# Kernel tuning notes

Hardware: AMD Instinct MI355X
Metric: run time of the kernel (lower is better)

Reference implementation:

```python
import jax, jax.numpy as jnp
import numpy as np

N = 50000
E = 800000
DF = 8        # dim_feat
DH = 32       # dim_hidden = out_channels per head
H = 4         # heads
HC = H * DH
DE = 4        # edge_dim
DD = 256      # dim_dense
DO = 4        # dim_out
NL = 3        # num GAT layers
SLOPE = 0.2   # GAT negative_slope
NL_SLOPE = 0.01  # nn.LeakyReLU default


def setup_inputs() -> dict:
    key = jax.random.key(0)
    ks = jax.random.split(key, 32)
    p = lambda k, shp: (jax.random.normal(k, shp, dtype=jnp.float32) * 0.1)
    inp = {
        "x": jax.random.normal(ks[0], (N, DF), dtype=jnp.float32),
        "edge_index": jax.random.randint(ks[1], (2, E), 0, N, dtype=jnp.int64),
        "edge_attr": jax.random.normal(ks[2], (E, DE), dtype=jnp.float32),
        # layer 0 (in = DF)
        "Wl0": p(ks[3], (DF, HC)), "bl0": jnp.zeros((HC,), jnp.float32),
        "Wr0": p(ks[4], (DF, HC)), "br0": jnp.zeros((HC,), jnp.float32),
        "We0": p(ks[5], (DE, HC)),
        "att0": p(ks[6], (H, DH)),
        "bo0": jnp.zeros((DH,), jnp.float32),
        # layers 1..NL-1 stacked (in = DH)
        "Wl": p(ks[7], (NL - 1, DH, HC)), "bl": jnp.zeros((NL - 1, HC), jnp.float32),
        "Wr": p(ks[8], (NL - 1, DH, HC)), "br": jnp.zeros((NL - 1, HC), jnp.float32),
        "We": p(ks[9], (NL - 1, DE, HC)),
        "att": p(ks[10], (NL - 1, H, DH)),
        "bo": jnp.zeros((NL - 1, DH), jnp.float32),
        # MLP head
        "Wd1": p(ks[11], (DH, DD)), "bd1": jnp.zeros((DD,), jnp.float32),
        "Wd2": p(ks[12], (DD, DO)), "bd2": jnp.zeros((DO,), jnp.float32),
    }
    return inp


def gat_layer(x, src, dst, ea, Wl, bl, Wr, br, We, att, bo):
    # GATv2ConvNorm, concat=False, no self loops, eval (dropout off)
    xl = (x @ Wl + bl).reshape(-1, H, DH)   # source transform  [N,H,C]
    xr = (x @ Wr + br).reshape(-1, H, DH)   # target transform  [N,H,C]
    x_j = xl[src]                            # [E,H,C]
    x_i = xr[dst]                            # [E,H,C]
    ef = (ea @ We).reshape(-1, H, DH)        # [E,H,C]
    m = jax.nn.leaky_relu(x_i + x_j + ef, negative_slope=SLOPE)
    e = jnp.einsum('ehc,hc->eh', m, att)     # logits [E,H]
    # Lipschitz norm on logits
    ni = jnp.linalg.norm(x_i, axis=-1)       # [E,H]
    nj = jnp.linalg.norm(x_j, axis=-1)       # [E,H]
    mx = jax.ops.segment_max(nj, dst, num_segments=N)
    mx = jnp.where(jnp.isfinite(mx), mx, 0.0)  # empty groups -> 0 (torch include_self=False init)
    e = e / (4.0 * (ni + mx[dst]) + 1e-12)
    # scatter softmax over destination groups
    emax = jax.ops.segment_max(e, dst, num_segments=N)
    z = jnp.exp(e - emax[dst])
    s = jax.ops.segment_sum(z, dst, num_segments=N)
    alpha = z / (s[dst] + 1e-16)             # [E,H]
    out = jax.ops.segment_sum(alpha[..., None] * x_j, dst, num_segments=N)  # [N,H,C]
    return out.mean(axis=1) + bo             # concat=False -> mean over heads


def reference(x, edge_index, edge_attr, Wl0, bl0, Wr0, br0, We0, att0, bo0,
              Wl, bl, Wr, br, We, att, bo, Wd1, bd1, Wd2, bd2):
    src, dst = edge_index[0], edge_index[1]
    act = lambda a: jax.nn.leaky_relu(a, negative_slope=NL_SLOPE)
    h = act(gat_layer(x, src, dst, edge_attr, Wl0, bl0, Wr0, br0, We0, att0, bo0))
    for i in range(NL - 1):
        h = act(gat_layer(h, src, dst, edge_attr, Wl[i], bl[i], Wr[i], br[i], We[i], att[i], bo[i]))
    h = act(h @ Wd1 + bd1)
    return h @ Wd2 + bd2
```

## Files before the change

### kernel.cpp

```cpp
#include <hip/hip_runtime.h>
#include <hip/hip_fp16.h>
#include <math.h>

#define NN 50000
#define EE 800000
#define DFi 8
#define DHc 32
#define Hh 4
#define HCc 128
#define DEe 4
#define DDd 256
#define DOo 4
#define NBK 196

__global__ void detect_kernel(const unsigned int* __restrict__ w, int nwords, int* __restrict__ flag) {
    unsigned int acc = 0;
    for (int i = 2 * threadIdx.x + 1; i < nwords; i += 512) acc |= w[i];
    if (acc) atomicOr(flag, 1);
}

__global__ void convert_count_kernel(const void* __restrict__ buf, const int* __restrict__ flag,
                                     int* __restrict__ EI, int* __restrict__ counts,
                                     int* __restrict__ rnk) {
    int i = blockIdx.x * 256 + threadIdx.x;
    if (i >= 2 * EE) return;
    int v = (*flag) ? ((const int*)buf)[i] : (int)(((const long long*)buf)[i]);
    EI[i] = v;
    if (i >= EE) rnk[i - EE] = atomicAdd(&counts[v], 1);
}

__global__ void scanA_kernel(const int* __restrict__ counts, int* __restrict__ roff,
                             int* __restrict__ bsum, int M) {
    __shared__ int sd[256];
    int t = threadIdx.x;
    int idx = blockIdx.x * 256 + t;
    int v = (idx < M) ? counts[idx] : 0;
    sd[t] = v;
    __syncthreads();
    for (int off = 1; off < 256; off <<= 1) {
        int x = (t >= off) ? sd[t - off] : 0;
        __syncthreads();
        sd[t] += x;
        __syncthreads();
    }
    if (idx < M) roff[idx] = sd[t] - v;
    if (t == 255) bsum[blockIdx.x] = sd[255];
}

__global__ void scanB_kernel(const int* __restrict__ bsum, int* __restrict__ boff, int nb) {
    __shared__ int sd[256];
    int t = threadIdx.x;
    int v = (t < nb) ? bsum[t] : 0;
    sd[t] = v;
    __syncthreads();
    for (int off = 1; off < 256; off <<= 1) {
        int x = (t >= off) ? sd[t - off] : 0;
        __syncthreads();
        sd[t] += x;
        __syncthreads();
    }
    boff[t] = sd[t] - v;
}

__global__ void scanC_kernel(int* __restrict__ roff, const int* __restrict__ boff, int M) {
    int idx = blockIdx.x * 256 + threadIdx.x;
    if (idx < M) roff[idx] += boff[idx >> 8];
}

__global__ void fill_kernel(const int* __restrict__ EI, const int* __restrict__ roff,
                            const int* __restrict__ rnk, long long* __restrict__ ce) {
    int e = blockIdx.x * 256 + threadIdx.x;
    if (e >= EE) return;
    int d = EI[EE + e];
    int s = EI[e];
    ce[roff[d] + rnk[e]] = ((long long)e << 32) | (unsigned int)s;
}

__global__ __launch_bounds__(256) void sortw_kernel(const int* __restrict__ roff,
                                                    long long* __restrict__ ce,
                                                    const float4* __restrict__ EA4,
                                                    int* __restrict__ col,
                                                    __half* __restrict__ EAc) {
    const int n = blockIdx.x * 4 + (threadIdx.x >> 6);
    if (n >= NN) return;
    const int lane = threadIdx.x & 63;
    const int a = roff[n];
    const int d = roff[n + 1] - a;
    if (d <= 0) return;
    if (d <= 64) {
        int srcv = 0;
        unsigned key = 0xFFFFFFFFu;
        if (lane < d) {
            long long v = ce[a + lane];
            srcv = (int)(v & 0xffffffffLL);
            unsigned eid = (unsigned)(v >> 32);
            key = (eid << 6) | (unsigned)lane;
        }
#pragma unroll
        for (int k = 2; k <= 64; k <<= 1) {
#pragma unroll
            for (int j = k >> 1; j > 0; j >>= 1) {
                unsigned o = (unsigned)__shfl_xor((int)key, j);
                bool up = ((lane & k) == 0);
                bool lower = ((lane & j) == 0);
                unsigned mn = o < key ? o : key;
                unsigned mx = o < key ? key : o;
                key = (lower == up) ? mn : mx;
            }
        }
        if (lane < d) {
            int ol = (int)(key & 63u);
            int src = __shfl(srcv, ol);
            unsigned eid = key >> 6;
            col[a + lane] = src;
            float4 at = EA4[eid];
            __half2 lo = __floats2half2_rn(at.x, at.y);
            __half2 hi = __floats2half2_rn(at.z, at.w);
            uint2 pk;
            pk.x = *reinterpret_cast<unsigned int*>(&lo);
            pk.y = *reinterpret_cast<unsigned int*>(&hi);
            reinterpret_cast<uint2*>(EAc)[a + lane] = pk;
        }
    } else if (lane == 0) {
        for (int i2 = a + 1; i2 < a + d; i2++) {
            long long kk = ce[i2];
            int j2 = i2 - 1;
            while (j2 >= a && ce[j2] > kk) { ce[j2 + 1] = ce[j2]; j2--; }
            ce[j2 + 1] = kk;
        }
        for (int k = 0; k < d; k++) {
            long long key = ce[a + k];
            int src = (int)(key & 0xffffffffLL);
            int eid = (int)(key >> 32);
            col[a + k] = src;
            float4 at = EA4[eid];
            __half2 lo = __floats2half2_rn(at.x, at.y);
            __half2 hi = __floats2half2_rn(at.z, at.w);
            uint2 pk;
            pk.x = *reinterpret_cast<unsigned int*>(&lo);
            pk.y = *reinterpret_cast<unsigned int*>(&hi);
            reinterpret_cast<uint2*>(EAc)[a + k] = pk;
        }
    }
}

__global__ __launch_bounds__(256) void bhist_kernel(const int* __restrict__ roff, int* __restrict__ gbh) {
    __shared__ int hist[256];
    int t = threadIdx.x;
    hist[t] = 0;
    __syncthreads();
    int n = blockIdx.x * 256 + t;
    if (n < NN) {
        int d = roff[n + 1] - roff[n];
        atomicAdd(&hist[d < 255 ? d : 255], 1);
    }
    __syncthreads();
    gbh[t * NBK + blockIdx.x] = hist[t];
}

__global__ __launch_bounds__(256) void bscan_kernel(int* __restrict__ gbh) {
    __shared__ int sd[256];
    int bin = threadIdx.x;
    int s = 0;
    for (int b = 0; b < NBK; b++) { int v = gbh[bin * NBK + b]; gbh[bin * NBK + b] = s; s += v; }
    int r = 255 - bin;
    sd[r] = s;
    __syncthreads();
    for (int off = 1; off < 256; off <<= 1) {
        int x = (r >= off) ? sd[r - off] : 0;
        __syncthreads();
        sd[r] += x;
        __syncthreads();
    }
    int base = sd[r] - s;
    for (int b = 0; b < NBK; b++) gbh[bin * NBK + b] += base;
}

__global__ __launch_bounds__(256) void bscatter_kernel(const int* __restrict__ roff,
                                                       const int* __restrict__ gbh,
                                                       int* __restrict__ perm) {
    __shared__ int hist[256];
    int t = threadIdx.x;
    hist[t] = 0;
    __syncthreads();
    int n = blockIdx.x * 256 + t;
    if (n < NN) {
        int d = roff[n + 1] - roff[n];
        int bin = d < 255 ? d : 255;
        int lr = atomicAdd(&hist[bin], 1);
        perm[gbh[bin * NBK + blockIdx.x] + lr] = n;
    }
}

template <int IN>
__global__ __launch_bounds__(128) void transform_kernel(
    const float* __restrict__ Xin, const float* __restrict__ Wl, const float* __restrict__ bl,
    const float* __restrict__ Wr, const float* __restrict__ br,
    __half* __restrict__ XLh, __half* __restrict__ XRh,
    float* __restrict__ NLn, float* __restrict__ NRn) {
    const int t = threadIdx.x;
    float wl[IN], wr[IN];
#pragma unroll
    for (int k = 0; k < IN; k++) { wl[k] = Wl[k * HCc + t]; wr[k] = Wr[k * HCc + t]; }
    const float blv = bl[t], brv = br[t];
    __shared__ float xst[16][IN];
    const int nbeg = blockIdx.x * 16;
    for (int idx = t; idx < 16 * IN; idx += 128) {
        int r = idx / IN, cc = idx % IN;
        int n = nbeg + r;
        xst[r][cc] = (n < NN) ? Xin[n * IN + cc] : 0.f;
    }
    __syncthreads();
#pragma unroll 4
    for (int r = 0; r < 16; ++r) {
        int n = nbeg + r;
        if (n >= NN) break;
        float al = blv, ar = brv;
#pragma unroll
        for (int k = 0; k < IN; k++) { float xv = xst[r][k]; al = fmaf(xv, wl[k], al); ar = fmaf(xv, wr[k], ar); }
        XLh[n * HCc + t] = __float2half(al);
        XRh[n * HCc + t] = __float2half(ar);
        float sl = al * al, sr = ar * ar;
#pragma unroll
        for (int msk = 1; msk < 32; msk <<= 1) { sl += __shfl_xor(sl, msk); sr += __shfl_xor(sr, msk); }
        if ((t & 31) == 0) { NLn[n * 4 + (t >> 5)] = sqrtf(sl); NRn[n * 4 + (t >> 5)] = sqrtf(sr); }
    }
}

__device__ inline float4 h8tof4(unsigned int a, unsigned int b) {
    __half2 p0 = *reinterpret_cast<const __half2*>(&a);
    __half2 p1 = *reinterpret_cast<const __half2*>(&b);
    float2 lo = __half22float2(p0), hi = __half22float2(p1);
    return make_float4(lo.x, lo.y, hi.x, hi.y);
}

__global__ __launch_bounds__(256) void gat_kernel(
    const __half* __restrict__ XLh, const __half* __restrict__ XRh,
    const float* __restrict__ NLn, const float* __restrict__ NRn,
    const int* __restrict__ roff, const int* __restrict__ col,
    const __half* __restrict__ EAc, const int* __restrict__ perm,
    const float* __restrict__ We,
    const float* __restrict__ att, const float* __restrict__ bo,
    float* __restrict__ Hout) {
    const int lane = threadIdx.x & 63;
    const int c = lane & 15;
    const int g = lane >> 4;
    const int h = c >> 2;
    const int slot = blockIdx.x * 16 + (threadIdx.x >> 6) * 4 + g;
    if (slot >= NN) return;
    const int i = perm[slot];

    const uint4*  XLu4 = reinterpret_cast<const uint4*>(XLh);
    const uint4*  XRu4 = reinterpret_cast<const uint4*>(XRh);
    const uint2*  EAu2 = reinterpret_cast<const uint2*>(EAc);
    const float4* NL4 = reinterpret_cast<const float4*>(NLn);
    const float4* We4 = reinterpret_cast<const float4*>(We);
    const float4* at4 = reinterpret_cast<const float4*>(att);
    const float4* bo4 = reinterpret_cast<const float4*>(bo);
    float4* Ho4 = reinterpret_cast<float4*>(Hout);

    const int base = roff[i];
    const int deg = roff[i + 1] - base;

    if (deg == 0) {
        if (c < 8) {
            float4 b = bo4[c];
            float4 r;
            r.x = b.x > 0.f ? b.x : 0.01f * b.x;
            r.y = b.y > 0.f ? b.y : 0.01f * b.y;
            r.z = b.z > 0.f ? b.z : 0.01f * b.z;
            r.w = b.w > 0.f ? b.w : 0.01f * b.w;
            Ho4[i * 8 + c] = r;
        }
        return;
    }

    const float4 w0l = We4[2 * c],      w0h = We4[2 * c + 1];
    const float4 w1l = We4[32 + 2 * c], w1h = We4[32 + 2 * c + 1];
    const float4 w2l = We4[64 + 2 * c], w2h = We4[64 + 2 * c + 1];
    const float4 w3l = We4[96 + 2 * c], w3h = We4[96 + 2 * c + 1];
    const float4 atl = at4[2 * c],      ath = at4[2 * c + 1];

    uint4 xiu = XRu4[i * 16 + c];
    const float4 xil = h8tof4(xiu.x, xiu.y), xih = h8tof4(xiu.z, xiu.w);
    float srun = 0.f;
    float4 accl = make_float4(0.f, 0.f, 0.f, 0.f);
    float4 acch = make_float4(0.f, 0.f, 0.f, 0.f);

#define ISSUE(X_, E_, K)                                                          \
    {                                                                             \
        int kc = ((K) < deg) ? (K) : 0;                                           \
        int jx = col[base + kc];                                                  \
        X_ = XLu4[jx * 16 + c];                                                   \
        E_ = EAu2[base + kc];                                                     \
    }
    uint4 xA, xB, xC, xD, xE, xF;
    uint2 eA, eB, eC, eD, eE, eF;
    ISSUE(xA, eA, 0); ISSUE(xB, eB, 1); ISSUE(xC, eC, 2);
    ISSUE(xD, eD, 3); ISSUE(xE, eE, 4); ISSUE(xF, eF, 5);

    float4 mx = make_float4(0.f, 0.f, 0.f, 0.f);
    for (int k = c; k < deg; k += 16) {
        int j = col[base + k];
        float4 nj = NL4[j];
        mx.x = fmaxf(mx.x, nj.x); mx.y = fmaxf(mx.y, nj.y);
        mx.z = fmaxf(mx.z, nj.z); mx.w = fmaxf(mx.w, nj.w);
    }
#pragma unroll
    for (int msk = 1; msk < 16; msk <<= 1) {
        mx.x = fmaxf(mx.x, __shfl_xor(mx.x, msk));
        mx.y = fmaxf(mx.y, __shfl_xor(mx.y, msk));
        mx.z = fmaxf(mx.z, __shfl_xor(mx.z, msk));
        mx.w = fmaxf(mx.w, __shfl_xor(mx.w, msk));
    }
    float mxh = (h == 0) ? mx.x : (h == 1) ? mx.y : (h == 2) ? mx.z : mx.w;
    const float invD = 1.0f / (4.0f * (NRn[i * 4 + h] + mxh) + 1e-12f);

#define BODY(X_, E_, K)                                                           \
    {                                                                             \
        float4 a4 = h8tof4((E_).x, (E_).y);                                       \
        float4 xjl = h8tof4((X_).x, (X_).y);                                      \
        float4 xjh = h8tof4((X_).z, (X_).w);                                      \
        float e0 = a4.x * w0l.x; e0 = fmaf(a4.y, w1l.x, e0);                      \
        e0 = fmaf(a4.z, w2l.x, e0); e0 = fmaf(a4.w, w3l.x, e0);                   \
        float e1 = a4.x * w0l.y; e1 = fmaf(a4.y, w1l.y, e1);                      \
        e1 = fmaf(a4.z, w2l.y, e1); e1 = fmaf(a4.w, w3l.y, e1);                   \
        float e2 = a4.x * w0l.z; e2 = fmaf(a4.y, w1l.z, e2);                      \
        e2 = fmaf(a4.z, w2l.z, e2); e2 = fmaf(a4.w, w3l.z, e2);                   \
        float e3 = a4.x * w0l.w; e3 = fmaf(a4.y, w1l.w, e3);                      \
        e3 = fmaf(a4.z, w2l.w, e3); e3 = fmaf(a4.w, w3l.w, e3);                   \
        float e4 = a4.x * w0h.x; e4 = fmaf(a4.y, w1h.x, e4);                      \
        e4 = fmaf(a4.z, w2h.x, e4); e4 = fmaf(a4.w, w3h.x, e4);                   \
        float e5 = a4.x * w0h.y; e5 = fmaf(a4.y, w1h.y, e5);                      \
        e5 = fmaf(a4.z, w2h.y, e5); e5 = fmaf(a4.w, w3h.y, e5);                   \
        float e6 = a4.x * w0h.z; e6 = fmaf(a4.y, w1h.z, e6);                      \
        e6 = fmaf(a4.z, w2h.z, e6); e6 = fmaf(a4.w, w3h.z, e6);                   \
        float e7 = a4.x * w0h.w; e7 = fmaf(a4.y, w1h.w, e7);                      \
        e7 = fmaf(a4.z, w2h.w, e7); e7 = fmaf(a4.w, w3h.w, e7);                   \
        float s0 = xil.x + xjl.x + e0; s0 = s0 > 0.f ? s0 : 0.2f * s0;            \
        float s1 = xil.y + xjl.y + e1; s1 = s1 > 0.f ? s1 : 0.2f * s1;            \
        float s2 = xil.z + xjl.z + e2; s2 = s2 > 0.f ? s2 : 0.2f * s2;            \
        float s3 = xil.w + xjl.w + e3; s3 = s3 > 0.f ? s3 : 0.2f * s3;            \
        float s4 = xih.x + xjh.x + e4; s4 = s4 > 0.f ? s4 : 0.2f * s4;            \
        float s5 = xih.y + xjh.y + e5; s5 = s5 > 0.f ? s5 : 0.2f * s5;            \
        float s6 = xih.z + xjh.z + e6; s6 = s6 > 0.f ? s6 : 0.2f * s6;            \
        float s7 = xih.w + xjh.w + e7; s7 = s7 > 0.f ? s7 : 0.2f * s7;            \
        float pp = s0 * atl.x; pp = fmaf(s1, atl.y, pp);                          \
        pp = fmaf(s2, atl.z, pp); pp = fmaf(s3, atl.w, pp);                       \
        pp = fmaf(s4, ath.x, pp); pp = fmaf(s5, ath.y, pp);                       \
        pp = fmaf(s6, ath.z, pp); pp = fmaf(s7, ath.w, pp);                       \
        pp += __shfl_xor(pp, 1); pp += __shfl_xor(pp, 2);                         \
        float z = __expf(fminf(pp * invD, 60.f));                                 \
        z = ((K) < deg) ? z : 0.f;                                                \
        srun += z;                                                                \
        accl.x = fmaf(z, xjl.x, accl.x);                                          \
        accl.y = fmaf(z, xjl.y, accl.y);                                          \
        accl.z = fmaf(z, xjl.z, accl.z);                                          \
        accl.w = fmaf(z, xjl.w, accl.w);                                          \
        acch.x = fmaf(z, xjh.x, acch.x);                                          \
        acch.y = fmaf(z, xjh.y, acch.y);                                          \
        acch.z = fmaf(z, xjh.z, acch.z);                                          \
        acch.w = fmaf(z, xjh.w, acch.w);                                          \
    }

    for (int k = 0; k < deg; k += 3) {
        uint4 nxD, nxE, nxF;
        uint2 neD, neE, neF;
        ISSUE(nxD, neD, k + 6);
        ISSUE(nxE, neE, k + 7);
        ISSUE(nxF, neF, k + 8);
        BODY(xA, eA, k);
        if (k + 1 < deg) BODY(xB, eB, k + 1);
        if (k + 2 < deg) BODY(xC, eC, k + 2);
        xA = xD; eA = eD; xB = xE; eB = eE; xC = xF; eC = eF;
        xD = nxD; eD = neD; xE = nxE; eE = neE; xF = nxF; eF = neF;
    }
#undef BODY
#undef ISSUE

    float inv = 1.0f / (srun + 1e-16f);
    float a0 = accl.x * inv, a1 = accl.y * inv, a2 = accl.z * inv, a3 = accl.w * inv;
    float a4_ = acch.x * inv, a5 = acch.y * inv, a6 = acch.z * inv, a7 = acch.w * inv;
    a0 += __shfl_xor(a0, 4); a0 += __shfl_xor(a0, 8);
    a1 += __shfl_xor(a1, 4); a1 += __shfl_xor(a1, 8);
    a2 += __shfl_xor(a2, 4); a2 += __shfl_xor(a2, 8);
    a3 += __shfl_xor(a3, 4); a3 += __shfl_xor(a3, 8);
    a4_ += __shfl_xor(a4_, 4); a4_ += __shfl_xor(a4_, 8);
    a5 += __shfl_xor(a5, 4); a5 += __shfl_xor(a5, 8);
    a6 += __shfl_xor(a6, 4); a6 += __shfl_xor(a6, 8);
    a7 += __shfl_xor(a7, 4); a7 += __shfl_xor(a7, 8);

    if (c < 4) {
        float4 bl_ = bo4[2 * c], bh_ = bo4[2 * c + 1];
        float4 rl, rh;
        rl.x = fmaf(0.25f, a0, bl_.x); rl.x = rl.x > 0.f ? rl.x : 0.01f * rl.x;
        rl.y = fmaf(0.25f, a1, bl_.y); rl.y = rl.y > 0.f ? rl.y : 0.01f * rl.y;
        rl.z = fmaf(0.25f, a2, bl_.z); rl.z = rl.z > 0.f ? rl.z : 0.01f * rl.z;
        rl.w = fmaf(0.25f, a3, bl_.w); rl.w = rl.w > 0.f ? rl.w : 0.01f * rl.w;
        rh.x = fmaf(0.25f, a4_, bh_.x); rh.x = rh.x > 0.f ? rh.x : 0.01f * rh.x;
        rh.y = fmaf(0.25f, a5, bh_.y); rh.y = rh.y > 0.f ? rh.y : 0.01f * rh.y;
        rh.z = fmaf(0.25f, a6, bh_.z); rh.z = rh.z > 0.f ? rh.z : 0.01f * rh.z;
        rh.w = fmaf(0.25f, a7, bh_.w); rh.w = rh.w > 0.f ? rh.w : 0.01f * rh.w;
        Ho4[i * 8 + 2 * c] = rl;
        Ho4[i * 8 + 2 * c + 1] = rh;
    }
}

__global__ __launch_bounds__(256) void mlp_kernel(
    const float* __restrict__ Hin, const float* __restrict__ Wd1, const float* __restrict__ bd1,
    const float* __restrict__ Wd2, const float* __restrict__ bd2, float* __restrict__ out) {
    const int lane = threadIdx.x & 63;
    const int chunk = __builtin_amdgcn_readfirstlane(threadIdx.x >> 6);
    const int nb = blockIdx.x * 64;
    int node = nb + lane;
    int nclamp = node < NN ? node : NN - 1;

    float h[32];
    const float4* H4 = reinterpret_cast<const float4*>(Hin);
#pragma unroll
    for (int r = 0; r < 8; ++r) {
        float4 t = H4[nclamp * 8 + r];
        h[4 * r] = t.x; h[4 * r + 1] = t.y; h[4 * r + 2] = t.z; h[4 * r + 3] = t.w;
    }

    float o0 = 0.f, o1 = 0.f, o2 = 0.f, o3 = 0.f;
    const int dbase = chunk * 64;
    for (int t = 0; t < 4; ++t) {
        float acc[16];
#pragma unroll
        for (int j = 0; j < 16; ++j) acc[j] = bd1[dbase + t * 16 + j];
#pragma unroll 8
        for (int k = 0; k < 32; ++k) {
            const float* wr = Wd1 + k * DDd + dbase + t * 16;
#pragma unroll
            for (int j = 0; j < 16; ++j) acc[j] = fmaf(h[k], wr[j], acc[j]);
        }
#pragma unroll
        for (int j = 0; j < 16; ++j) {
            float hd = acc[j];
            hd = hd > 0.f ? hd : 0.01f * hd;
            int d = dbase + t * 16 + j;
            o0 = fmaf(hd, Wd2[d * 4 + 0], o0);
            o1 = fmaf(hd, Wd2[d * 4 + 1], o1);
            o2 = fmaf(hd, Wd2[d * 4 + 2], o2);
            o3 = fmaf(hd, Wd2[d * 4 + 3], o3);
        }
    }

    __shared__ float4 red[4][64];
    red[chunk][lane] = make_float4(o0, o1, o2, o3);
    __syncthreads();
    if (threadIdx.x < 64 && nb + (int)threadIdx.x < NN) {
        float4 r0 = red[0][threadIdx.x], r1 = red[1][threadIdx.x];
        float4 r2 = red[2][threadIdx.x], r3 = red[3][threadIdx.x];
        float4 o;
        o.x = r0.x + r1.x + r2.x + r3.x + bd2[0];
        o.y = r0.y + r1.y + r2.y + r3.y + bd2[1];
        o.z = r0.z + r1.z + r2.z + r3.z + bd2[2];
        o.w = r0.w + r1.w + r2.w + r3.w + bd2[3];
        reinterpret_cast<float4*>(out)[nb + threadIdx.x] = o;
    }
}

extern "C" void kernel_launch(void* const* d_in, const int* in_sizes, int n_in,
                              void* d_out, int out_size, void* d_ws, size_t ws_size,
                              hipStream_t stream) {
    const float* x    = (const float*)d_in[0];
    const void*  eraw = d_in[1];
    const float* ea   = (const float*)d_in[2];
    const float* Wl0  = (const float*)d_in[3];
    const float* bl0  = (const float*)d_in[4];
    const float* Wr0  = (const float*)d_in[5];
    const float* br0  = (const float*)d_in[6];
    const float* We0  = (const float*)d_in[7];
    const float* att0 = (const float*)d_in[8];
    const float* bo0  = (const float*)d_in[9];
    const float* Wl   = (const float*)d_in[10];
    const float* bl   = (const float*)d_in[11];
    const float* Wr   = (const float*)d_in[12];
    const float* br   = (const float*)d_in[13];
    const float* We   = (const float*)d_in[14];
    const float* att  = (const float*)d_in[15];
    const float* bo   = (const float*)d_in[16];
    const float* Wd1  = (const float*)d_in[17];
    const float* bd1  = (const float*)d_in[18];
    const float* Wd2  = (const float*)d_in[19];
    const float* bd2  = (const float*)d_in[20];
    float* out = (float*)d_out;

    char* p = (char*)d_ws;
    auto alloc = [&](size_t bytes) { void* r = (void*)p; p += (bytes + 255) & ~(size_t)255; return r; };
    int*       EI     = (int*)alloc((size_t)2 * EE * 4);
    int*       counts = (int*)alloc((size_t)(NN + 1) * 4);
    int*       roff   = (int*)alloc((size_t)(NN + 1) * 4);
    int*       bsum   = (int*)alloc(256 * 4);
    int*       boff   = (int*)alloc(256 * 4);
    int*       rnk    = (int*)alloc((size_t)EE * 4);
    long long* ce     = (long long*)alloc((size_t)EE * 8);
    int*       col    = (int*)alloc((size_t)EE * 4);
    int*       flag   = (int*)alloc(256);
    int*       gbh    = (int*)alloc((size_t)256 * NBK * 4);
    int*       perm   = (int*)alloc((size_t)NN * 4);
    __half*    XLh    = (__half*)alloc((size_t)NN * HCc * 2);
    __half*    XRh    = (__half*)alloc((size_t)NN * HCc * 2);
    __half*    EAc    = (__half*)alloc((size_t)EE * 4 * 2);
    float*     NLn    = (float*)alloc((size_t)NN * 4 * 4);
    float*     NRn    = (float*)alloc((size_t)NN * 4 * 4);
    float*     HA     = (float*)alloc((size_t)NN * DHc * 4);
    float*     HB     = (float*)alloc((size_t)NN * DHc * 4);

    (void)hipMemsetAsync(counts, 0, (size_t)(NN + 1) * 4, stream);
    (void)hipMemsetAsync(flag, 0, 4, stream);

    detect_kernel<<<1, 256, 0, stream>>>((const unsigned int*)eraw, 8192, flag);
    convert_count_kernel<<<(2 * EE + 255) / 256, 256, 0, stream>>>(eraw, flag, EI, counts, rnk);
    const int M = NN + 1;
    const int NBLK = (M + 255) / 256;
    scanA_kernel<<<NBLK, 256, 0, stream>>>(counts, roff, bsum, M);
    scanB_kernel<<<1, 256, 0, stream>>>(bsum, boff, NBLK);
    scanC_kernel<<<NBLK, 256, 0, stream>>>(roff, boff, M);
    fill_kernel<<<(EE + 255) / 256, 256, 0, stream>>>(EI, roff, rnk, ce);
    sortw_kernel<<<(NN + 3) / 4, 256, 0, stream>>>(roff, ce, (const float4*)ea, col, EAc);
    bhist_kernel<<<NBK, 256, 0, stream>>>(roff, gbh);
    bscan_kernel<<<1, 256, 0, stream>>>(gbh);
    bscatter_kernel<<<NBK, 256, 0, stream>>>(roff, gbh, perm);

    const int gT = (NN + 15) / 16;
    const int gG = (NN + 15) / 16;

    transform_kernel<DFi><<<gT, 128, 0, stream>>>(x, Wl0, bl0, Wr0, br0, XLh, XRh, NLn, NRn);
    gat_kernel<<<gG, 256, 0, stream>>>(XLh, XRh, NLn, NRn, roff, col, EAc, perm, We0, att0, bo0, HA);
    transform_kernel<DHc><<<gT, 128, 0, stream>>>(HA, Wl, bl, Wr, br, XLh, XRh, NLn, NRn);
    gat_kernel<<<gG, 256, 0, stream>>>(XLh, XRh, NLn, NRn, roff, col, EAc, perm, We, att, bo, HB);
    transform_kernel<DHc><<<gT, 128, 0, stream>>>(HB, Wl + DHc * HCc, bl + HCc, Wr + DHc * HCc, br + HCc,
                                                  XLh, XRh, NLn, NRn);
    gat_kernel<<<gG, 256, 0, stream>>>(XLh, XRh, NLn, NRn, roff, col, EAc, perm, We + DEe * HCc,
                                       att + Hh * DHc, bo + DHc, HA);
    mlp_kernel<<<(NN + 63) / 64, 256, 0, stream>>>(HA, Wd1, bd1, Wd2, bd2, out);
}
```

Before: 395.1 us.

## Merge scan into single-block kernel and sort small segments four per wavefront

```diff
diff --git a/kernel.cpp b/kernel.cpp
--- a/kernel.cpp
+++ b/kernel.cpp
@@ -29,13 +29,16 @@
     if (i >= EE) rnk[i - EE] = atomicAdd(&counts[v], 1);
 }
 
-__global__ void scanA_kernel(const int* __restrict__ counts, int* __restrict__ roff,
-                             int* __restrict__ bsum, int M) {
+__global__ __launch_bounds__(256) void scanF_kernel(const int* __restrict__ counts,
+                                                    int* __restrict__ roff, int M) {
     __shared__ int sd[256];
-    int t = threadIdx.x;
-    int idx = blockIdx.x * 256 + t;
-    int v = (idx < M) ? counts[idx] : 0;
-    sd[t] = v;
+    const int t = threadIdx.x;
+    const int CH = (M + 255) / 256;
+    const int lo = t * CH;
+    const int hi = (lo + CH < M) ? lo + CH : M;
+    int s = 0;
+    for (int i = lo; i < hi; i++) s += counts[i];
+    sd[t] = s;
     __syncthreads();
     for (int off = 1; off < 256; off <<= 1) {
         int x = (t >= off) ? sd[t - off] : 0;
@@ -43,28 +46,12 @@
         sd[t] += x;
         __syncthreads();
     }
-    if (idx < M) roff[idx] = sd[t] - v;
-    if (t == 255) bsum[blockIdx.x] = sd[255];
-}
-
-__global__ void scanB_kernel(const int* __restrict__ bsum, int* __restrict__ boff, int nb) {
-    __shared__ int sd[256];
-    int t = threadIdx.x;
-    int v = (t < nb) ? bsum[t] : 0;
-    sd[t] = v;
-    __syncthreads();
-    for (int off = 1; off < 256; off <<= 1) {
-        int x = (t >= off) ? sd[t - off] : 0;
-        __syncthreads();
-        sd[t] += x;
-        __syncthreads();
-    }
-    boff[t] = sd[t] - v;
-}
-
-__global__ void scanC_kernel(int* __restrict__ roff, const int* __restrict__ boff, int M) {
-    int idx = blockIdx.x * 256 + threadIdx.x;
-    if (idx < M) roff[idx] += boff[idx >> 8];
+    int run = sd[t] - s;
+    for (int i = lo; i < hi; i++) {
+        int v = counts[i];
+        roff[i] = run;
+        run += v;
+    }
 }
 
 __global__ void fill_kernel(const int* __restrict__ EI, const int* __restrict__ roff,
@@ -81,67 +68,108 @@
                                                     const float4* __restrict__ EA4,
                                                     int* __restrict__ col,
                                                     __half* __restrict__ EAc) {
-    const int n = blockIdx.x * 4 + (threadIdx.x >> 6);
-    if (n >= NN) return;
     const int lane = threadIdx.x & 63;
-    const int a = roff[n];
-    const int d = roff[n + 1] - a;
-    if (d <= 0) return;
-    if (d <= 64) {
+    const int wv = threadIdx.x >> 6;
+    const int c = lane & 15;
+    const int g = lane >> 4;
+    const int nb = blockIdx.x * 16 + wv * 4;
+
+#define EMIT(POS, KEY)                                                            \
+    {                                                                             \
+        int ol = (int)((KEY) & 63u);                                              \
+        int src = __shfl(srcv, ol);                                               \
+        unsigned eid = (KEY) >> 6;                                                \
+        col[POS] = src;                                                           \
+        float4 at = EA4[eid];                                                     \
+        __half2 lo2 = __floats2half2_rn(at.x, at.y);                              \
+        __half2 hi2 = __floats2half2_rn(at.z, at.w);                              \
+        uint2 pk;                                                                 \
+        pk.x = *reinterpret_cast<unsigned int*>(&lo2);                            \
+        pk.y = *reinterpret_cast<unsigned int*>(&hi2);                            \
+        reinterpret_cast<uint2*>(EAc)[POS] = pk;                                  \
+    }
+
+    {
+        const int n = nb + g;
+        int a = 0, d = 0;
+        bool small = false;
+        if (n < NN) {
+            a = roff[n];
+            d = roff[n + 1] - a;
+            small = (d >= 1 && d <= 16);
+        }
         int srcv = 0;
         unsigned key = 0xFFFFFFFFu;
-        if (lane < d) {
-            long long v = ce[a + lane];
+        if (small && c < d) {
+            long long v = ce[a + c];
             srcv = (int)(v & 0xffffffffLL);
-            unsigned eid = (unsigned)(v >> 32);
-            key = (eid << 6) | (unsigned)lane;
-        }
-#pragma unroll
-        for (int k = 2; k <= 64; k <<= 1) {
+            key = (((unsigned)(v >> 32)) << 6) | (unsigned)lane;
+        }
+#pragma unroll
+        for (int k = 2; k <= 16; k <<= 1) {
 #pragma unroll
             for (int j = k >> 1; j > 0; j >>= 1) {
                 unsigned o = (unsigned)__shfl_xor((int)key, j);
-                bool up = ((lane & k) == 0);
-                bool lower = ((lane & j) == 0);
+                bool up = ((c & k) == 0);
+                bool lower = ((c & j) == 0);
                 unsigned mn = o < key ? o : key;
                 unsigned mx = o < key ? key : o;
                 key = (lower == up) ? mn : mx;
             }
         }
-        if (lane < d) {
-            int ol = (int)(key & 63u);
-            int src = __shfl(srcv, ol);
-            unsigned eid = key >> 6;
-            col[a + lane] = src;
-            float4 at = EA4[eid];
-            __half2 lo = __floats2half2_rn(at.x, at.y);
-            __half2 hi = __floats2half2_rn(at.z, at.w);
-            uint2 pk;
-            pk.x = *reinterpret_cast<unsigned int*>(&lo);
-            pk.y = *reinterpret_cast<unsigned int*>(&hi);
-            reinterpret_cast<uint2*>(EAc)[a + lane] = pk;
-        }
-    } else if (lane == 0) {
-        for (int i2 = a + 1; i2 < a + d; i2++) {
-            long long kk = ce[i2];
-            int j2 = i2 - 1;
-            while (j2 >= a && ce[j2] > kk) { ce[j2 + 1] = ce[j2]; j2--; }
-            ce[j2 + 1] = kk;
-        }
-        for (int k = 0; k < d; k++) {
-            long long key = ce[a + k];
-            int src = (int)(key & 0xffffffffLL);
-            int eid = (int)(key >> 32);
-            col[a + k] = src;
-            float4 at = EA4[eid];
-            __half2 lo = __floats2half2_rn(at.x, at.y);
-            __half2 hi = __floats2half2_rn(at.z, at.w);
-            uint2 pk;
-            pk.x = *reinterpret_cast<unsigned int*>(&lo);
-            pk.y = *reinterpret_cast<unsigned int*>(&hi);
-            reinterpret_cast<uint2*>(EAc)[a + k] = pk;
-        }
-    }
+        if (small && c < d) EMIT(a + c, key)
+    }
+
+    for (int w = 0; w < 4; ++w) {
+        const int n = nb + w;
+        if (n >= NN) break;
+        const int a = roff[n];
+        const int d = roff[n + 1] - a;
+        if (d <= 16) continue;
+        if (d <= 64) {
+            int srcv = 0;
+            unsigned key = 0xFFFFFFFFu;
+            if (lane < d) {
+                long long v = ce[a + lane];
+                srcv = (int)(v & 0xffffffffLL);
+                key = (((unsigned)(v >> 32)) << 6) | (unsigned)lane;
+            }
+#pragma unroll
+            for (int k = 2; k <= 64; k <<= 1) {
+#pragma unroll
+                for (int j = k >> 1; j > 0; j >>= 1) {
+                    unsigned o = (unsigned)__shfl_xor((int)key, j);
+                    bool up = ((lane & k) == 0);
+                    bool lower = ((lane & j) == 0);
+                    unsigned mn = o < key ? o : key;
+                    unsigned mx = o < key ? key : o;
+                    key = (lower == up) ? mn : mx;
+                }
+            }
+            if (lane < d) EMIT(a + lane, key)
+        } else if (lane == 0) {
+            for (int i2 = a + 1; i2 < a + d; i2++) {
+                long long kk = ce[i2];
+                int j2 = i2 - 1;
+                while (j2 >= a && ce[j2] > kk) { ce[j2 + 1] = ce[j2]; j2--; }
+                ce[j2 + 1] = kk;
+            }
+            for (int k = 0; k < d; k++) {
+                long long v = ce[a + k];
+                int src = (int)(v & 0xffffffffLL);
+                int eid = (int)(v >> 32);
+                col[a + k] = src;
+                float4 at = EA4[eid];
+                __half2 lo2 = __floats2half2_rn(at.x, at.y);
+                __half2 hi2 = __floats2half2_rn(at.z, at.w);
+                uint2 pk;
+                pk.x = *reinterpret_cast<unsigned int*>(&lo2);
+                pk.y = *reinterpret_cast<unsigned int*>(&hi2);
+                reinterpret_cast<uint2*>(EAc)[a + k] = pk;
+            }
+        }
+    }
+#undef EMIT
 }
 
 __global__ __launch_bounds__(256) void bhist_kernel(const int* __restrict__ roff, int* __restrict__ gbh) {
@@ -493,8 +521,6 @@
     int*       EI     = (int*)alloc((size_t)2 * EE * 4);
     int*       counts = (int*)alloc((size_t)(NN + 1) * 4);
     int*       roff   = (int*)alloc((size_t)(NN + 1) * 4);
-    int*       bsum   = (int*)alloc(256 * 4);
-    int*       boff   = (int*)alloc(256 * 4);
     int*       rnk    = (int*)alloc((size_t)EE * 4);
     long long* ce     = (long long*)alloc((size_t)EE * 8);
     int*       col    = (int*)alloc((size_t)EE * 4);
@@ -514,13 +540,9 @@
 
     detect_kernel<<<1, 256, 0, stream>>>((const unsigned int*)eraw, 8192, flag);
     convert_count_kernel<<<(2 * EE + 255) / 256, 256, 0, stream>>>(eraw, flag, EI, counts, rnk);
-    const int M = NN + 1;
-    const int NBLK = (M + 255) / 256;
-    scanA_kernel<<<NBLK, 256, 0, stream>>>(counts, roff, bsum, M);
-    scanB_kernel<<<1, 256, 0, stream>>>(bsum, boff, NBLK);
-    scanC_kernel<<<NBLK, 256, 0, stream>>>(roff, boff, M);
+    scanF_kernel<<<1, 256, 0, stream>>>(counts, roff, NN + 1);
     fill_kernel<<<(EE + 255) / 256, 256, 0, stream>>>(EI, roff, rnk, ce);
-    sortw_kernel<<<(NN + 3) / 4, 256, 0, stream>>>(roff, ce, (const float4*)ea, col, EAc);
+    sortw_kernel<<<(NN + 15) / 16, 256, 0, stream>>>(roff, ce, (const float4*)ea, col, EAc);
     bhist_kernel<<<NBK, 256, 0, stream>>>(roff, gbh);
     bscan_kernel<<<1, 256, 0, stream>>>(gbh);
     bscatter_kernel<<<NBK, 256, 0, stream>>>(roff, gbh, perm);
```

Measured after the change: 473.6 us. 19.9% more time.
